# Optimization experiments

Measured on AMD Instinct MI355X. Metric: run time of the kernel, lower is better.

Reference implementation:

```python
import jax, jax.numpy as jnp
import numpy as np

D_MODEL = 1024
NUM_HEADS = 16
HEAD_DIM = D_MODEL // NUM_HEADS


def setup_inputs() -> dict:
    key = jax.random.key(0)
    ks = jax.random.split(key, 10)
    s = 1.0 / np.sqrt(D_MODEL)
    x = jax.random.normal(ks[0], (2, 2048, D_MODEL), dtype=jnp.float32)
    mask = jax.random.randint(ks[1], (1, 1, 2048, 2048), 0, 2, dtype=jnp.int32)
    Wq = jax.random.uniform(ks[2], (D_MODEL, D_MODEL), jnp.float32, -s, s)
    bq = jnp.zeros((D_MODEL,), jnp.float32)
    Wk = jax.random.uniform(ks[3], (D_MODEL, D_MODEL), jnp.float32, -s, s)
    bk = jnp.zeros((D_MODEL,), jnp.float32)
    Wv = jax.random.uniform(ks[4], (D_MODEL, D_MODEL), jnp.float32, -s, s)
    bv = jnp.zeros((D_MODEL,), jnp.float32)
    Wo = jax.random.uniform(ks[5], (D_MODEL, D_MODEL), jnp.float32, -s, s)
    bo = jnp.zeros((D_MODEL,), jnp.float32)
    return {"x": x, "mask": mask, "Wq": Wq, "bq": bq, "Wk": Wk, "bk": bk,
            "Wv": Wv, "bv": bv, "Wo": Wo, "bo": bo}


def reference(x, mask, Wq, bq, Wk, bk, Wv, bv, Wo, bo):
    B, S, D = x.shape
    # Q/K/V projections, split into heads: [B, H, S, Dh]
    q = (x @ Wq + bq).reshape(B, S, NUM_HEADS, HEAD_DIM).transpose(0, 2, 1, 3)
    k = (x @ Wk + bk).reshape(B, S, NUM_HEADS, HEAD_DIM).transpose(0, 2, 1, 3)
    v = (x @ Wv + bv).reshape(B, S, NUM_HEADS, HEAD_DIM).transpose(0, 2, 1, 3)
    # scores: [B, H, S, S]
    scores = jnp.einsum('bhqd,bhkd->bhqk', q, k) / np.sqrt(HEAD_DIM).astype(np.float32)
    scores = jnp.where(mask == 0, jnp.float32(-1e9), scores)
    weights = jax.nn.softmax(scores, axis=-1)
    # dropout is identity in eval / p=0
    context = jnp.einsum('bhqk,bhkd->bhqd', weights, v)
    context = context.transpose(0, 2, 1, 3).reshape(B, S, D)
    return context @ Wo + bo
```

## Files before the change

### kernel.cpp

```cpp
#include <hip/hip_runtime.h>
#include <stdint.h>

typedef unsigned short u16;
typedef unsigned int u32;
typedef u16 u16x4 __attribute__((ext_vector_type(4)));
typedef u16 u16x8 __attribute__((ext_vector_type(8)));
typedef __bf16 bf16x8 __attribute__((ext_vector_type(8)));
typedef float f32x4 __attribute__((ext_vector_type(4)));

#define GLL16(g, l) __builtin_amdgcn_global_load_lds( \
    (const __attribute__((address_space(1))) void*)(g), \
    (__attribute__((address_space(3))) void*)(l), 16, 0, 0)

__device__ __forceinline__ u16 f2bf(float f) {
  u32 u = __builtin_bit_cast(u32, f);
  u += 0x7fffu + ((u >> 16) & 1u);
  return (u16)(u >> 16);
}
__device__ __forceinline__ bf16x8 asbf(u16x8 v) { return __builtin_bit_cast(bf16x8, v); }

__global__ void k_cvt_x(const float* __restrict__ x, u16* __restrict__ o) {
  int i = blockIdx.x * 256 + threadIdx.x;
  f32x4 v = ((const f32x4*)x)[i];
  u16x4 r = { f2bf(v[0]), f2bf(v[1]), f2bf(v[2]), f2bf(v[3]) };
  ((u16x4*)o)[i] = r;
}

__global__ void k_cvt_wT(const float* __restrict__ w, u16* __restrict__ wt, float scale) {
  __shared__ float t[32][33];
  int k0 = blockIdx.x << 5, n0 = blockIdx.y << 5;
  int lx = threadIdx.x & 31, ly = threadIdx.x >> 5;
  #pragma unroll
  for (int i = 0; i < 4; ++i)
    t[ly + 8*i][lx] = w[(size_t)(k0 + ly + 8*i) * 1024 + n0 + lx];
  __syncthreads();
  #pragma unroll
  for (int i = 0; i < 4; ++i)
    wt[(size_t)(n0 + ly + 8*i) * 1024 + k0 + lx] = f2bf(t[lx][ly + 8*i] * scale);
}

__global__ void k_bias(const float* __restrict__ bq, const float* __restrict__ bk,
                       const float* __restrict__ bv, float* __restrict__ o) {
  int i = blockIdx.x * 256 + threadIdx.x;
  float v;
  if (i < 1024) v = bq[i] * 0.125f;
  else if (i < 2048) v = bk[i - 1024];
  else v = bv[i - 2048];
  o[i] = v;
}

__global__ void k_maskbits(const int* __restrict__ mask, u32* __restrict__ bits) {
  int w = blockIdx.x * 256 + threadIdx.x;
  const int* src = mask + (size_t)w * 32;
  u32 b = 0;
  #pragma unroll
  for (int i = 0; i < 32; ++i) b |= (src[i] != 0 ? 1u : 0u) << i;
  bits[w] = b;
}

template<int EPI>
__global__ __launch_bounds__(256)
void k_gemm(const u16* __restrict__ A, const u16* __restrict__ Bt,
            const float* __restrict__ bias, float* __restrict__ outF,
            u16* __restrict__ qws, u16* __restrict__ kws, u16* __restrict__ vtws)
{
  __shared__ u16 As[128 * 32];
  __shared__ u16 Bs[128 * 32];
  const int tid = threadIdx.x;
  const int lane = tid & 63;
  const int wv = tid >> 6;
  const int g = lane >> 4, cc = lane & 15;
  const int wr = wv >> 1, wc = wv & 1;
  const int bm = blockIdx.y, bn = blockIdx.x;

  f32x4 acc[4][4] = {};

  for (int k0 = 0; k0 < 1024; k0 += 32) {
    __syncthreads();
    #pragma unroll
    for (int call = 0; call < 2; ++call) {
      int idx = call * 256 + tid;
      int row = idx >> 2;
      int sw = ((idx & 3) << 4) ^ ((row & 3) << 4);
      GLL16((const char*)(A + (size_t)(bm * 128 + row) * 1024 + k0) + sw,
            (char*)As + (call * 256 + wv * 64) * 16);
      GLL16((const char*)(Bt + (size_t)(bn * 128 + row) * 1024 + k0) + sw,
            (char*)Bs + (call * 256 + wv * 64) * 16);
    }
    __syncthreads();

    u16x8 a[4], b[4];
    #pragma unroll
    for (int m = 0; m < 4; ++m) {
      int row = wr * 64 + m * 16 + cc;
      a[m] = *(const u16x8*)((const char*)As + row * 64 + ((g * 16) ^ ((row & 3) << 4)));
    }
    #pragma unroll
    for (int n = 0; n < 4; ++n) {
      int row = wc * 64 + n * 16 + cc;
      b[n] = *(const u16x8*)((const char*)Bs + row * 64 + ((g * 16) ^ ((row & 3) << 4)));
    }
    #pragma unroll
    for (int m = 0; m < 4; ++m)
      #pragma unroll
      for (int n = 0; n < 4; ++n)
        acc[m][n] = __builtin_amdgcn_mfma_f32_16x16x32_bf16(asbf(a[m]), asbf(b[n]), acc[m][n], 0, 0, 0);
  }

  if constexpr (EPI == 1) {
    #pragma unroll
    for (int m = 0; m < 4; ++m) {
      int Mrow0 = bm * 128 + wr * 64 + m * 16 + g * 4;
      #pragma unroll
      for (int n = 0; n < 4; ++n) {
        int Ncol = bn * 128 + wc * 64 + n * 16 + cc;
        float bvv = bias[Ncol];
        #pragma unroll
        for (int r = 0; r < 4; ++r)
          outF[(size_t)(Mrow0 + r) * 1024 + Ncol] = acc[m][n][r] + bvv;
      }
    }
  } else {
    #pragma unroll
    for (int n = 0; n < 4; ++n) {
      int Ncol = bn * 128 + wc * 64 + n * 16 + cc;
      float bvv = bias[Ncol];
      int which = Ncol >> 10;
      int h = (Ncol >> 6) & 15;
      int d = Ncol & 63;
      #pragma unroll
      for (int m = 0; m < 4; ++m) {
        int Mrow0 = bm * 128 + wr * 64 + m * 16 + g * 4;
        int bb = Mrow0 >> 11;
        int s0 = Mrow0 & 2047;
        int bh = bb * 16 + h;
        if (which == 0) {
          u16* dst = qws + ((size_t)bh * 2048 + s0) * 64 + d;
          #pragma unroll
          for (int r = 0; r < 4; ++r) dst[(size_t)r * 64] = f2bf(acc[m][n][r] + bvv);
        } else if (which == 1) {
          u16* dst = kws + ((size_t)bh * 2048 + s0) * 64 + d;
          #pragma unroll
          for (int r = 0; r < 4; ++r) dst[(size_t)r * 64] = f2bf(acc[m][n][r] + bvv);
        } else {
          u16* dst = vtws + ((size_t)bh * 64 + d) * 2048 + s0;
          #pragma unroll
          for (int r = 0; r < 4; ++r) dst[r] = f2bf(acc[m][n][r] + bvv);
        }
      }
    }
  }
}

__global__ __launch_bounds__(256)
void k_attn(const u16* __restrict__ qws, const u16* __restrict__ kws,
            const u16* __restrict__ vtws, const u32* __restrict__ mbits,
            u16* __restrict__ ctx)
{
  __shared__ u16 Kt[64 * 64];
  __shared__ u16 Vt[64 * 64];
  __shared__ float Pl[4][16][68];

  const int tid = threadIdx.x;
  const int lane = tid & 63;
  const int wv = tid >> 6;
  const int g = lane >> 4;
  const int cc = lane & 15;
  const int blk = blockIdx.x;
  const int qc = blk & 31;
  const int bh = blk >> 5;
  const int b = bh >> 4, h = bh & 15;
  const size_t base = (size_t)bh * (2048 * 64);
  const int qrow = qc * 64 + wv * 16;
  const int qm0 = qrow + g * 4;

  u16x8 qf0, qf1;
  {
    const u16* qp = qws + base + (size_t)(qrow + cc) * 64 + g * 8;
    qf0 = *(const u16x8*)qp;
    qf1 = *(const u16x8*)(qp + 32);
  }

  f32x4 oacc[4] = {};
  float mrun[4] = {-1e30f, -1e30f, -1e30f, -1e30f};
  float lrun[4] = {0.f, 0.f, 0.f, 0.f};

  for (int kb = 0; kb < 2048; kb += 64) {
    __syncthreads();
    #pragma unroll
    for (int call = 0; call < 2; ++call) {
      int idx = call * 256 + tid;
      int row = idx >> 3;
      int sw = ((idx & 7) << 4) ^ ((row & 7) << 4);
      GLL16((const char*)(kws + base + (size_t)(kb + row) * 64) + sw,
            (char*)Kt + (call * 256 + wv * 64) * 16);
      GLL16((const char*)(vtws + base + (size_t)row * 2048 + kb) + sw,
            (char*)Vt + (call * 256 + wv * 64) * 16);
    }
    __syncthreads();

    u32 mw0[4], mw1[4];
    #pragma unroll
    for (int r = 0; r < 4; ++r) {
      const u32* mp = mbits + (size_t)(qm0 + r) * 64 + (kb >> 5);
      mw0[r] = mp[0];
      mw1[r] = mp[1];
    }

    f32x4 sc[4];
    #pragma unroll
    for (int t = 0; t < 4; ++t) {
      int row = t * 16 + cc;
      int swz = (row & 7) << 4;
      const char* kr = (const char*)Kt + row * 128;
      u16x8 kf0 = *(const u16x8*)(kr + ((g * 16) ^ swz));
      u16x8 kf1 = *(const u16x8*)(kr + ((g * 16 + 64) ^ swz));
      f32x4 s = {};
      s = __builtin_amdgcn_mfma_f32_16x16x32_bf16(asbf(qf0), asbf(kf0), s, 0, 0, 0);
      s = __builtin_amdgcn_mfma_f32_16x16x32_bf16(asbf(qf1), asbf(kf1), s, 0, 0, 0);
      int bitpos = t * 16 + cc;
      int sh = bitpos & 31;
      #pragma unroll
      for (int r = 0; r < 4; ++r) {
        u32 w = (bitpos >> 5) ? mw1[r] : mw0[r];
        s[r] = ((w >> sh) & 1u) ? s[r] : -1e9f;
      }
      sc[t] = s;
    }

    float alpha[4];
    #pragma unroll
    for (int r = 0; r < 4; ++r) {
      float v = fmaxf(fmaxf(sc[0][r], sc[1][r]), fmaxf(sc[2][r], sc[3][r]));
      v = fmaxf(v, __shfl_xor(v, 1));
      v = fmaxf(v, __shfl_xor(v, 2));
      v = fmaxf(v, __shfl_xor(v, 4));
      v = fmaxf(v, __shfl_xor(v, 8));
      float mn = fmaxf(mrun[r], v);
      alpha[r] = __expf(mrun[r] - mn);
      mrun[r] = mn;
    }
    #pragma unroll
    for (int f = 0; f < 4; ++f)
      #pragma unroll
      for (int r = 0; r < 4; ++r)
        oacc[f][r] *= alpha[r];

    float rs[4] = {0.f, 0.f, 0.f, 0.f};
    #pragma unroll
    for (int t = 0; t < 4; ++t) {
      #pragma unroll
      for (int r = 0; r < 4; ++r) {
        float pvv = __expf(sc[t][r] - mrun[r]);
        rs[r] += pvv;
        Pl[wv][g * 4 + r][t * 16 + cc] = pvv;
      }
    }
    #pragma unroll
    for (int r = 0; r < 4; ++r) {
      float v = rs[r];
      v += __shfl_xor(v, 1);
      v += __shfl_xor(v, 2);
      v += __shfl_xor(v, 4);
      v += __shfl_xor(v, 8);
      lrun[r] = lrun[r] * alpha[r] + v;
    }

    asm volatile("s_waitcnt lgkmcnt(0)" ::: "memory");

    #pragma unroll
    for (int ch = 0; ch < 2; ++ch) {
      const float* pp = &Pl[wv][cc][g * 8 + ch * 32];
      f32x4 p0 = *(const f32x4*)pp;
      f32x4 p1 = *(const f32x4*)(pp + 4);
      u16x8 pa;
      pa[0] = f2bf(p0[0]); pa[1] = f2bf(p0[1]); pa[2] = f2bf(p0[2]); pa[3] = f2bf(p0[3]);
      pa[4] = f2bf(p1[0]); pa[5] = f2bf(p1[1]); pa[6] = f2bf(p1[2]); pa[7] = f2bf(p1[3]);
      #pragma unroll
      for (int f = 0; f < 4; ++f) {
        int row = f * 16 + cc;
        int swz = (row & 7) << 4;
        u16x8 vf = *(const u16x8*)((const char*)Vt + row * 128 + ((g * 16 + ch * 64) ^ swz));
        oacc[f] = __builtin_amdgcn_mfma_f32_16x16x32_bf16(asbf(pa), asbf(vf), oacc[f], 0, 0, 0);
      }
    }
  }

  float inv[4];
  #pragma unroll
  for (int r = 0; r < 4; ++r) inv[r] = 1.0f / lrun[r];
  #pragma unroll
  for (int f = 0; f < 4; ++f) {
    #pragma unroll
    for (int r = 0; r < 4; ++r) {
      int q = qrow + g * 4 + r;
      ctx[((size_t)(b * 2048 + q)) * 1024 + h * 64 + f * 16 + cc] = f2bf(oacc[f][r] * inv[r]);
    }
  }
}

extern "C" void kernel_launch(void* const* d_in, const int* in_sizes, int n_in,
                              void* d_out, int out_size, void* d_ws, size_t ws_size,
                              hipStream_t stream) {
  (void)in_sizes; (void)n_in; (void)out_size; (void)ws_size;
  const float* x   = (const float*)d_in[0];
  const int*  mask = (const int*)d_in[1];
  const float* Wq  = (const float*)d_in[2];
  const float* bq  = (const float*)d_in[3];
  const float* Wk  = (const float*)d_in[4];
  const float* bk  = (const float*)d_in[5];
  const float* Wv  = (const float*)d_in[6];
  const float* bv  = (const float*)d_in[7];
  const float* Wo  = (const float*)d_in[8];
  const float* bo  = (const float*)d_in[9];

  char* p = (char*)d_ws;
  size_t off = 0;
  auto carve = [&](size_t n) { char* r = p + off; off = (off + n + 255) & ~(size_t)255; return r; };
  u16*  xb    = (u16*)carve((size_t)4096 * 1024 * 2);
  u16*  wqkvt = (u16*)carve((size_t)3072 * 1024 * 2);
  u16*  wot   = (u16*)carve((size_t)1024 * 1024 * 2);
  float* bqkv = (float*)carve(3072 * 4);
  u32*  mbits = (u32*)carve((size_t)2048 * 64 * 4);
  u16*  qws   = (u16*)carve((size_t)32 * 2048 * 64 * 2);
  u16*  kws   = (u16*)carve((size_t)32 * 2048 * 64 * 2);
  u16*  vtws  = (u16*)carve((size_t)32 * 2048 * 64 * 2);
  u16*  ctx   = (u16*)carve((size_t)4096 * 1024 * 2);

  k_cvt_x<<<dim3(4096), dim3(256), 0, stream>>>(x, xb);
  k_cvt_wT<<<dim3(32, 32), dim3(256), 0, stream>>>(Wq, wqkvt, 0.125f);
  k_cvt_wT<<<dim3(32, 32), dim3(256), 0, stream>>>(Wk, wqkvt + 1024 * 1024, 1.0f);
  k_cvt_wT<<<dim3(32, 32), dim3(256), 0, stream>>>(Wv, wqkvt + 2 * 1024 * 1024, 1.0f);
  k_cvt_wT<<<dim3(32, 32), dim3(256), 0, stream>>>(Wo, wot, 1.0f);
  k_bias<<<dim3(12), dim3(256), 0, stream>>>(bq, bk, bv, bqkv);
  k_maskbits<<<dim3(512), dim3(256), 0, stream>>>(mask, mbits);

  k_gemm<0><<<dim3(24, 32), dim3(256), 0, stream>>>(xb, wqkvt, bqkv, nullptr, qws, kws, vtws);
  k_attn<<<dim3(1024), dim3(256), 0, stream>>>(qws, kws, vtws, mbits, ctx);
  k_gemm<1><<<dim3(8, 32), dim3(256), 0, stream>>>(ctx, wot, bo, (float*)d_out, nullptr, nullptr, nullptr);
}
```

Before: 303.0 us.

## Double-buffer K/V tiles and keep softmax probabilities in registers via transposed MFMA

The attention kernel now double-buffers the K and V shared-memory tiles, issuing the async global-to-LDS loads for the next block before computing the current one, so there is one barrier per iteration instead of two. The QK^T MFMA operands are swapped and K rows are permuted at staging, so each lane holds a full query's scores. That lets P be packed to bf16 with v_cvt_pk_bf16_f32 and fed straight into the PV MFMA, removing the LDS round-trip through the Pl buffer. The max and sum reductions shrink to two cross-lane shuffles, and alpha is redistributed with __shfl; launch bounds are also tightened to 4 blocks, which may raise register pressure.

```diff
diff --git a/kernel.cpp b/kernel.cpp
--- a/kernel.cpp
+++ b/kernel.cpp
@@ -5,6 +5,7 @@
 typedef unsigned int u32;
 typedef u16 u16x4 __attribute__((ext_vector_type(4)));
 typedef u16 u16x8 __attribute__((ext_vector_type(8)));
+typedef u32 u32x4 __attribute__((ext_vector_type(4)));
 typedef __bf16 bf16x8 __attribute__((ext_vector_type(8)));
 typedef float f32x4 __attribute__((ext_vector_type(4)));
 
@@ -152,14 +153,13 @@
   }
 }
 
-__global__ __launch_bounds__(256)
+__global__ __launch_bounds__(256, 4)
 void k_attn(const u16* __restrict__ qws, const u16* __restrict__ kws,
             const u16* __restrict__ vtws, const u32* __restrict__ mbits,
             u16* __restrict__ ctx)
 {
-  __shared__ u16 Kt[64 * 64];
-  __shared__ u16 Vt[64 * 64];
-  __shared__ float Pl[4][16][68];
+  __shared__ u16 Kt[2][64 * 64];
+  __shared__ u16 Vt[2][64 * 64];
 
   const int tid = threadIdx.x;
   const int lane = tid & 63;
@@ -172,7 +172,6 @@
   const int b = bh >> 4, h = bh & 15;
   const size_t base = (size_t)bh * (2048 * 64);
   const int qrow = qc * 64 + wv * 16;
-  const int qm0 = qrow + g * 4;
 
   u16x8 qf0, qf1;
   {
@@ -180,123 +179,133 @@
     qf0 = *(const u16x8*)qp;
     qf1 = *(const u16x8*)(qp + 32);
   }
+  const u32* mq = mbits + (size_t)(qrow + cc) * 64;
 
   f32x4 oacc[4] = {};
-  float mrun[4] = {-1e30f, -1e30f, -1e30f, -1e30f};
-  float lrun[4] = {0.f, 0.f, 0.f, 0.f};
-
-  for (int kb = 0; kb < 2048; kb += 64) {
-    __syncthreads();
+  float mrun = -1e30f, lrun = 0.f;
+
+  auto STAGE = [&](int bufi, int kb) {
     #pragma unroll
     for (int call = 0; call < 2; ++call) {
       int idx = call * 256 + tid;
       int row = idx >> 3;
       int sw = ((idx & 7) << 4) ^ ((row & 7) << 4);
-      GLL16((const char*)(kws + base + (size_t)(kb + row) * 64) + sw,
-            (char*)Kt + (call * 256 + wv * 64) * 16);
+      int krow = (row & 32) + (((row >> 2) & 3) << 3) + (((row >> 4) & 1) << 2) + (row & 3);
+      GLL16((const char*)(kws + base + (size_t)(kb + krow) * 64) + sw,
+            (char*)&Kt[bufi][0] + (call * 256 + wv * 64) * 16);
       GLL16((const char*)(vtws + base + (size_t)row * 2048 + kb) + sw,
-            (char*)Vt + (call * 256 + wv * 64) * 16);
-    }
-    __syncthreads();
-
-    u32 mw0[4], mw1[4];
-    #pragma unroll
-    for (int r = 0; r < 4; ++r) {
-      const u32* mp = mbits + (size_t)(qm0 + r) * 64 + (kb >> 5);
-      mw0[r] = mp[0];
-      mw1[r] = mp[1];
-    }
+            (char*)&Vt[bufi][0] + (call * 256 + wv * 64) * 16);
+    }
+  };
+
+  STAGE(0, 0);
+  __syncthreads();
+
+  int cur = 0;
+  for (int kb = 0; kb < 2048; kb += 64) {
+    if (kb + 64 < 2048) STAGE(cur ^ 1, kb + 64);
+
+    uint2 mw2 = *(const uint2*)(mq + (kb >> 5));
+    u32 m0 = mw2.x >> (g * 8);
+    u32 m1 = mw2.y >> (g * 8);
 
     f32x4 sc[4];
     #pragma unroll
     for (int t = 0; t < 4; ++t) {
       int row = t * 16 + cc;
       int swz = (row & 7) << 4;
-      const char* kr = (const char*)Kt + row * 128;
+      const char* kr = (const char*)&Kt[cur][0] + row * 128;
       u16x8 kf0 = *(const u16x8*)(kr + ((g * 16) ^ swz));
       u16x8 kf1 = *(const u16x8*)(kr + ((g * 16 + 64) ^ swz));
       f32x4 s = {};
-      s = __builtin_amdgcn_mfma_f32_16x16x32_bf16(asbf(qf0), asbf(kf0), s, 0, 0, 0);
-      s = __builtin_amdgcn_mfma_f32_16x16x32_bf16(asbf(qf1), asbf(kf1), s, 0, 0, 0);
-      int bitpos = t * 16 + cc;
-      int sh = bitpos & 31;
+      s = __builtin_amdgcn_mfma_f32_16x16x32_bf16(asbf(kf0), asbf(qf0), s, 0, 0, 0);
+      s = __builtin_amdgcn_mfma_f32_16x16x32_bf16(asbf(kf1), asbf(qf1), s, 0, 0, 0);
+      sc[t] = s;
+    }
+
+    #pragma unroll
+    for (int t = 0; t < 4; ++t) {
+      u32 msel = (t >> 1) ? m1 : m0;
       #pragma unroll
       for (int r = 0; r < 4; ++r) {
-        u32 w = (bitpos >> 5) ? mw1[r] : mw0[r];
-        s[r] = ((w >> sh) & 1u) ? s[r] : -1e9f;
-      }
-      sc[t] = s;
-    }
-
-    float alpha[4];
-    #pragma unroll
-    for (int r = 0; r < 4; ++r) {
-      float v = fmaxf(fmaxf(sc[0][r], sc[1][r]), fmaxf(sc[2][r], sc[3][r]));
-      v = fmaxf(v, __shfl_xor(v, 1));
-      v = fmaxf(v, __shfl_xor(v, 2));
-      v = fmaxf(v, __shfl_xor(v, 4));
-      v = fmaxf(v, __shfl_xor(v, 8));
-      float mn = fmaxf(mrun[r], v);
-      alpha[r] = __expf(mrun[r] - mn);
-      mrun[r] = mn;
-    }
+        u32 bit = (msel >> (4 * (t & 1) + r)) & 1u;
+        sc[t][r] = bit ? sc[t][r] : -1e9f;
+      }
+    }
+
+    float vmax;
+    {
+      f32x4 m4;
+      #pragma unroll
+      for (int r = 0; r < 4; ++r)
+        m4[r] = fmaxf(fmaxf(sc[0][r], sc[1][r]), fmaxf(sc[2][r], sc[3][r]));
+      vmax = fmaxf(fmaxf(m4[0], m4[1]), fmaxf(m4[2], m4[3]));
+      vmax = fmaxf(vmax, __shfl_xor(vmax, 16));
+      vmax = fmaxf(vmax, __shfl_xor(vmax, 32));
+    }
+    float mn = fmaxf(mrun, vmax);
+    float alpha = __expf(mrun - mn);
+    mrun = mn;
+
+    float rs = 0.f;
+    #pragma unroll
+    for (int t = 0; t < 4; ++t)
+      #pragma unroll
+      for (int r = 0; r < 4; ++r) {
+        float pv = __expf(sc[t][r] - mn);
+        sc[t][r] = pv;
+        rs += pv;
+      }
+    u32 pk[8];
+    #pragma unroll
+    for (int t = 0; t < 4; ++t) {
+      u32 w0, w1;
+      asm("v_cvt_pk_bf16_f32 %0, %1, %2" : "=v"(w0) : "v"(sc[t][0]), "v"(sc[t][1]));
+      asm("v_cvt_pk_bf16_f32 %0, %1, %2" : "=v"(w1) : "v"(sc[t][2]), "v"(sc[t][3]));
+      pk[2 * t] = w0;
+      pk[2 * t + 1] = w1;
+    }
+    rs += __shfl_xor(rs, 16);
+    rs += __shfl_xor(rs, 32);
+    lrun = lrun * alpha + rs;
+
+    float a_o[4];
+    #pragma unroll
+    for (int r = 0; r < 4; ++r) a_o[r] = __shfl(alpha, 4 * g + r);
     #pragma unroll
     for (int f = 0; f < 4; ++f)
       #pragma unroll
       for (int r = 0; r < 4; ++r)
-        oacc[f][r] *= alpha[r];
-
-    float rs[4] = {0.f, 0.f, 0.f, 0.f};
-    #pragma unroll
-    for (int t = 0; t < 4; ++t) {
-      #pragma unroll
-      for (int r = 0; r < 4; ++r) {
-        float pvv = __expf(sc[t][r] - mrun[r]);
-        rs[r] += pvv;
-        Pl[wv][g * 4 + r][t * 16 + cc] = pvv;
-      }
-    }
-    #pragma unroll
-    for (int r = 0; r < 4; ++r) {
-      float v = rs[r];
-      v += __shfl_xor(v, 1);
-      v += __shfl_xor(v, 2);
-      v += __shfl_xor(v, 4);
-      v += __shfl_xor(v, 8);
-      lrun[r] = lrun[r] * alpha[r] + v;
-    }
-
-    asm volatile("s_waitcnt lgkmcnt(0)" ::: "memory");
+        oacc[f][r] *= a_o[r];
 
     #pragma unroll
     for (int ch = 0; ch < 2; ++ch) {
-      const float* pp = &Pl[wv][cc][g * 8 + ch * 32];
-      f32x4 p0 = *(const f32x4*)pp;
-      f32x4 p1 = *(const f32x4*)(pp + 4);
-      u16x8 pa;
-      pa[0] = f2bf(p0[0]); pa[1] = f2bf(p0[1]); pa[2] = f2bf(p0[2]); pa[3] = f2bf(p0[3]);
-      pa[4] = f2bf(p1[0]); pa[5] = f2bf(p1[1]); pa[6] = f2bf(p1[2]); pa[7] = f2bf(p1[3]);
+      u32x4 pw = { pk[4 * ch], pk[4 * ch + 1], pk[4 * ch + 2], pk[4 * ch + 3] };
+      u16x8 pa = __builtin_bit_cast(u16x8, pw);
       #pragma unroll
       for (int f = 0; f < 4; ++f) {
         int row = f * 16 + cc;
         int swz = (row & 7) << 4;
-        u16x8 vf = *(const u16x8*)((const char*)Vt + row * 128 + ((g * 16 + ch * 64) ^ swz));
+        u16x8 vf = *(const u16x8*)((const char*)&Vt[cur][0] + row * 128 + ((g * 16 + ch * 64) ^ swz));
         oacc[f] = __builtin_amdgcn_mfma_f32_16x16x32_bf16(asbf(pa), asbf(vf), oacc[f], 0, 0, 0);
       }
     }
+
+    __syncthreads();
+    cur ^= 1;
   }
 
-  float inv[4];
-  #pragma unroll
-  for (int r = 0; r < 4; ++r) inv[r] = 1.0f / lrun[r];
-  #pragma unroll
-  for (int f = 0; f < 4; ++f) {
+  float inv = 1.0f / lrun;
+  float i_o[4];
+  #pragma unroll
+  for (int r = 0; r < 4; ++r) i_o[r] = __shfl(inv, 4 * g + r);
+  #pragma unroll
+  for (int f = 0; f < 4; ++f)
     #pragma unroll
     for (int r = 0; r < 4; ++r) {
-      int q = qrow + g * 4 + r;
-      ctx[((size_t)(b * 2048 + q)) * 1024 + h * 64 + f * 16 + cc] = f2bf(oacc[f][r] * inv[r]);
-    }
-  }
+      int q = qrow + 4 * g + r;
+      ctx[((size_t)(b * 2048 + q)) * 1024 + h * 64 + f * 16 + cc] = f2bf(oacc[f][r] * i_o[r]);
+    }
 }
 
 extern "C" void kernel_launch(void* const* d_in, const int* in_sizes, int n_in,
```

Result: faster. 263.0 us (-13.2%).
